# Optimization experiments

Measured on AMD Instinct MI355X. Metric: run time of the kernel, lower is better.

The kernel has to match this reference:

```python
import jax, jax.numpy as jnp
import numpy as np

N_NODES = 50000
N_EDGES = 640000
D = 128
L = 3


def setup_inputs() -> dict:
    key = jax.random.key(0)
    k1, k2, k3, k4 = jax.random.split(key, 4)
    x = jax.random.normal(k1, (N_NODES, D), dtype=jnp.float32)
    # Glorot-ish scale so activations stay O(1) across 3 layers
    Ws = jax.random.normal(k2, (L, D, D), dtype=jnp.float32) * (1.0 / np.sqrt(D))
    bs = jnp.zeros((L, D), dtype=jnp.float32)
    edge_src = jax.random.randint(k3, (N_EDGES,), 0, N_NODES, dtype=jnp.int32)
    edge_dst = jax.random.randint(k4, (N_EDGES,), 0, N_NODES, dtype=jnp.int32)
    return {"x": x, "Ws": Ws, "bs": bs, "edge_src": edge_src, "edge_dst": edge_dst}


def reference(x, Ws, bs, edge_src, edge_dst):
    n = x.shape[0]
    ones = jnp.ones(edge_src.shape[0], dtype=x.dtype)
    # degrees, clamped to 1 as in dgl GraphConv(norm='both')
    deg_out = jnp.maximum(jax.ops.segment_sum(ones, edge_src, num_segments=n), 1.0)
    deg_in = jnp.maximum(jax.ops.segment_sum(ones, edge_dst, num_segments=n), 1.0)
    inv_sqrt_out = jax.lax.rsqrt(deg_out)[:, None]  # [N,1]
    inv_sqrt_in = jax.lax.rsqrt(deg_in)[:, None]    # [N,1]
    for l in range(Ws.shape[0]):
        h = x * inv_sqrt_out                         # src normalization
        msg = h[edge_src]                            # [E,D] gather
        agg = jax.ops.segment_sum(msg, edge_dst, num_segments=n)  # [N,D] scatter-add
        h = agg * inv_sqrt_in                        # dst normalization
        x = jax.nn.relu(h @ Ws[l] + bs[l])           # linear + ReLU
    return x
```

## Files before the change

### kernel.cpp

```cpp
#include <hip/hip_runtime.h>
#include <hip/hip_fp16.h>

typedef __attribute__((ext_vector_type(8))) _Float16 half8;
typedef __attribute__((ext_vector_type(4))) float f32x4;
typedef unsigned int u32;
typedef unsigned short u16;
typedef unsigned long long u64;

#define ELL_PAD 64


__global__ __launch_bounds__(256) void initpack(int* __restrict__ deg_out,
                                                int* __restrict__ deg_in,
                                                u32* __restrict__ xz0,
                                                u32* __restrict__ xz1,
                                                const float* __restrict__ Ws,
                                                _Float16* __restrict__ Whi,
                                                _Float16* __restrict__ Wlo,
                                                int N, int padU32, int zb, int packTotal) {
  int b = blockIdx.x;
  if (b < zb) {
    int i = b * 256 + threadIdx.x;
    if (i < N) { deg_out[i] = 0; deg_in[i] = 0; }
    if (b == 0) {
      for (int j = threadIdx.x; j < padU32; j += 256) { xz0[j] = 0; xz1[j] = 0; }
    }
    return;
  }
  int i = (b - zb) * 256 + threadIdx.x;
  if (i < packTotal) {
    int lane  = i & 63;
    int kstep = (i >> 6) & 3;
    int ntile = (i >> 8) & 7;
    int layer = i >> 11;
    int nn = ntile * 16 + (lane & 15);
    int k0 = kstep * 32 + (lane >> 4) * 8;
    const float* W = Ws + (size_t)layer * 128 * 128;
    size_t base = (size_t)i * 8;
    for (int j = 0; j < 8; j++) {
      float v = W[(k0 + j) * 128 + nn];
      _Float16 hi = (_Float16)v;
      Whi[base + j] = hi;
      Wlo[base + j] = (_Float16)(v - (float)hi);
    }
  }
}


__global__ __launch_bounds__(256) void build(const int* __restrict__ esrc,
                                             const int* __restrict__ edst,
                                             int* __restrict__ deg_out,
                                             int* __restrict__ deg_in,
                                             u16* __restrict__ ell, int E) {
  int i = blockIdx.x * 256 + threadIdx.x;
  if (i >= E) return;
  int s = esrc[i];
  int d = edst[i];
  atomicAdd(&deg_out[s], 1);
  int p = atomicAdd(&deg_in[d], 1);
  if (p < ELL_PAD) ell[(u32)d * ELL_PAD + (u32)p] = (u16)s;
}


__global__ __launch_bounds__(256) void xscale(const float* __restrict__ x,
                                              const int* __restrict__ deg_out,
                                              const int* __restrict__ deg_in,
                                              __half2* __restrict__ xh,
                                              u16* __restrict__ ell,
                                              int N, int n64) {
  int gid = blockIdx.x * 256 + threadIdx.x;
  if (gid >= n64) return;
  int row = gid >> 6;
  int d = deg_out[row]; if (d < 1) d = 1;
  float s = rsqrtf((float)d);
  float2 v = ((const float2*)x)[gid];
  xh[gid] = __floats2half2_rn(v.x * s, v.y * s);
  if ((gid & 63) == 0) {
    int c = deg_in[row];
    int l = c > ELL_PAD ? ELL_PAD : c;
    int t = (l + 3) & ~3;
    u16* ep = ell + (u32)row * ELL_PAD;
    for (int q = l; q < t; q++) ep[q] = (u16)N;
  }
}


__global__ __launch_bounds__(512) void layer16(const _Float16* __restrict__ xh,
                                               const int* __restrict__ deg_in,
                                               const u16* __restrict__ ell,
                                               const _Float16* __restrict__ Whi,
                                               const _Float16* __restrict__ Wlo,
                                               const float* __restrict__ bias,
                                               const int* __restrict__ deg_out,
                                               __half* __restrict__ out16,
                                               float* __restrict__ out32, int n) {
  __shared__ _Float16 As[16 * 136];
  const int wave = threadIdx.x >> 6;
  const int lane = threadIdx.x & 63;
  const int sub  = lane & 15;
  const int grp  = lane >> 4;
  const int sh   = grp << 4;
  const u32 sub16 = (u32)sub * 16u;
  const int rowBase = blockIdx.x * 16;
  const char* __restrict__ xb = (const char*)xh;

  {
    int r0 = rowBase + wave * 2, r1 = r0 + 1;
    int d0 = (r0 < n) ? deg_in[r0] : 0;
    int d1 = (r1 < n) ? deg_in[r1] : 0;
    int l0 = d0 > ELL_PAD ? ELL_PAD : d0;
    int l1 = d1 > ELL_PAD ? ELL_PAD : d1;
    int t0 = (l0 + 3) & ~3;
    int t1 = (l1 + 3) & ~3;
    const u16* ep0 = ell + (u32)(r0 < n ? r0 : 0) * ELL_PAD;
    const u16* ep1 = ell + (u32)(r1 < n ? r1 : 0) * ELL_PAD;

    float a0[8] = {0.f, 0.f, 0.f, 0.f, 0.f, 0.f, 0.f, 0.f};
    float a1[8] = {0.f, 0.f, 0.f, 0.f, 0.f, 0.f, 0.f, 0.f};

    int m = t0 < t1 ? t0 : t1;
    int e = 0;
    for (; e + 8 <= m; e += 8) {
      u64 wa0 = *(const u64*)&ep0[e];
      u64 wa1 = *(const u64*)&ep0[e + 4];
      u64 wb0 = *(const u64*)&ep1[e];
      u64 wb1 = *(const u64*)&ep1[e + 4];
      u32 ia0 = ((u32)(wa0 >> sh) & 0xFFFFu) * 256u + sub16;
      u32 ia1 = ((u32)(wa1 >> sh) & 0xFFFFu) * 256u + sub16;
      u32 ib0 = ((u32)(wb0 >> sh) & 0xFFFFu) * 256u + sub16;
      u32 ib1 = ((u32)(wb1 >> sh) & 0xFFFFu) * 256u + sub16;
      half8 va0 = *(const half8*)(xb + ia0);
      half8 va1 = *(const half8*)(xb + ia1);
      half8 vb0 = *(const half8*)(xb + ib0);
      half8 vb1 = *(const half8*)(xb + ib1);
#pragma unroll
      for (int j = 0; j < 8; j++) {
        a0[j] += (float)va0[j] + (float)va1[j];
        a1[j] += (float)vb0[j] + (float)vb1[j];
      }
    }
    for (; e < m; e += 4) {
      u64 wa = *(const u64*)&ep0[e];
      u64 wb = *(const u64*)&ep1[e];
      u32 ia = ((u32)(wa >> sh) & 0xFFFFu) * 256u + sub16;
      u32 ib = ((u32)(wb >> sh) & 0xFFFFu) * 256u + sub16;
      half8 va = *(const half8*)(xb + ia);
      half8 vb = *(const half8*)(xb + ib);
#pragma unroll
      for (int j = 0; j < 8; j++) { a0[j] += (float)va[j]; a1[j] += (float)vb[j]; }
    }
    for (int ea = m; ea < t0; ea += 4) {
      u64 wa = *(const u64*)&ep0[ea];
      u32 ia = ((u32)(wa >> sh) & 0xFFFFu) * 256u + sub16;
      half8 va = *(const half8*)(xb + ia);
#pragma unroll
      for (int j = 0; j < 8; j++) a0[j] += (float)va[j];
    }
    for (int eb = m; eb < t1; eb += 4) {
      u64 wb = *(const u64*)&ep1[eb];
      u32 ib = ((u32)(wb >> sh) & 0xFFFFu) * 256u + sub16;
      half8 vb = *(const half8*)(xb + ib);
#pragma unroll
      for (int j = 0; j < 8; j++) a1[j] += (float)vb[j];
    }

#pragma unroll
    for (int j = 0; j < 8; j++) {
      a0[j] += __shfl_xor(a0[j], 16, 64);
      a0[j] += __shfl_xor(a0[j], 32, 64);
      a1[j] += __shfl_xor(a1[j], 16, 64);
      a1[j] += __shfl_xor(a1[j], 32, 64);
    }

    float si0 = rsqrtf((float)(d0 < 1 ? 1 : d0));
    float si1 = rsqrtf((float)(d1 < 1 ? 1 : d1));
    if (grp == 0) {
      half8 h0, h1;
#pragma unroll
      for (int j = 0; j < 8; j++) {
        h0[j] = (_Float16)(a0[j] * si0);
        h1[j] = (_Float16)(a1[j] * si1);
      }
      *(half8*)&As[(wave * 2 + 0) * 136 + sub * 8] = h0;
      *(half8*)&As[(wave * 2 + 1) * 136 + sub * 8] = h1;
    }
  }
  __syncthreads();

  f32x4 acc = (f32x4){0.f, 0.f, 0.f, 0.f};
#pragma unroll
  for (int ks = 0; ks < 4; ks++) {
    half8 a  = *(const half8*)&As[(size_t)sub * 136 + ks * 32 + grp * 8];
    half8 bh = *(const half8*)&Whi[((wave * 4 + ks) * 64 + lane) * 8];
    half8 bl = *(const half8*)&Wlo[((wave * 4 + ks) * 64 + lane) * 8];
    acc = __builtin_amdgcn_mfma_f32_16x16x32_f16(a, bh, acc, 0, 0, 0);
    acc = __builtin_amdgcn_mfma_f32_16x16x32_f16(a, bl, acc, 0, 0, 0);
  }

  const int r0c = rowBase + grp * 4;
  const int col = wave * 16 + sub;
  const float bv = bias[col];
#pragma unroll
  for (int r = 0; r < 4; r++) {
    int row = r0c + r;
    if (row < n) {
      float v = fmaxf(acc[r] + bv, 0.f);
      if (out16) {
        int d = deg_out[row]; if (d < 1) d = 1;
        out16[(size_t)row * 128 + col] = __float2half(v * rsqrtf((float)d));
      } else {
        out32[(size_t)row * 128 + col] = v;
      }
    }
  }
}


extern "C" void kernel_launch(void* const* d_in, const int* in_sizes, int n_in,
                              void* d_out, int out_size, void* d_ws, size_t ws_size,
                              hipStream_t stream) {
  const float* x   = (const float*)d_in[0];
  const float* Ws  = (const float*)d_in[1];
  const float* bs  = (const float*)d_in[2];
  const int* esrc  = (const int*)d_in[3];
  const int* edst  = (const int*)d_in[4];

  const int D = 128;
  const int N = in_sizes[0] / D;
  const int E = in_sizes[3];
  const int L = in_sizes[1] / (D * D);
  const int Npad = ((N + 15) / 16) * 16;

  char* base = (char*)d_ws;
  size_t off = 0;
  auto alloc = [&](size_t bytes) {
    char* p = base + off;
    off = (off + bytes + 255) & ~(size_t)255;
    return p;
  };
  int*      deg_out = (int*)alloc((size_t)N * 4);
  int*      deg_in  = (int*)alloc((size_t)N * 4);
  u16*      ell     = (u16*)alloc((size_t)N * ELL_PAD * 2);
  _Float16* Whi     = (_Float16*)alloc((size_t)L * 16384 * 2);
  _Float16* Wlo     = (_Float16*)alloc((size_t)L * 16384 * 2);
  _Float16* xh0     = (_Float16*)alloc((size_t)(Npad + 16) * 128 * 2);
  _Float16* xh1     = (_Float16*)alloc((size_t)(Npad + 16) * 128 * 2);

  const int zb = (N + 255) / 256;
  const int packTotal = L * 2048;
  const int packB = (packTotal + 255) / 256;
  const int padU32 = 16 * 64;

  initpack<<<dim3(zb + packB), dim3(256), 0, stream>>>(
      deg_out, deg_in,
      (u32*)(xh0 + (size_t)N * 128), (u32*)(xh1 + (size_t)N * 128),
      Ws, Whi, Wlo, N, padU32, zb, packTotal);
  build<<<dim3((E + 255) / 256), dim3(256), 0, stream>>>(
      esrc, edst, deg_out, deg_in, ell, E);
  xscale<<<dim3((N * 64 + 255) / 256), dim3(256), 0, stream>>>(
      x, deg_out, deg_in, (__half2*)xh0, ell, N, N * 64);

  float* outf = (float*)d_out;
  _Float16* ping[2] = {xh0, xh1};
  const dim3 lgrid(Npad / 16), lblk(512);

  for (int l = 0; l < L; l++) {
    bool last = (l == L - 1);
    layer16<<<lgrid, lblk, 0, stream>>>(
        (const _Float16*)ping[l & 1], deg_in, ell,
        Whi + (size_t)l * 16384, Wlo + (size_t)l * 16384,
        bs + (size_t)l * D, deg_out,
        last ? nullptr : (__half*)ping[(l + 1) & 1],
        last ? outf : nullptr, N);
  }
}
```

Baseline: 262.6 us.

## Build ELL adjacency via two-pass bucketed partition instead of global atomics

Replaces the single build kernel, which did global atomics on deg_in and scattered 16-bit ELL writes, with a two-pass partition. Pass one bins edges by destination bucket in shared memory and records per-block run offsets. Pass two assembles each 128-node bucket's ELL slice in LDS and writes it out coalesced, padding unused slots with N. This removes contended global atomics and scattered stores but adds an extra kernel, intermediate buffers and serial single-thread prefix scans.

New measurement: 250.8 us. -4.5%, faster.

```diff
diff --git a/kernel.cpp b/kernel.cpp
--- a/kernel.cpp
+++ b/kernel.cpp
@@ -8,10 +8,13 @@
 typedef unsigned long long u64;
 
 #define ELL_PAD 64
+#define BKT 128
+#define BKT_SH 7
+#define EPB 2048
+#define NAMAX 512
 
 
 __global__ __launch_bounds__(256) void initpack(int* __restrict__ deg_out,
-                                                int* __restrict__ deg_in,
                                                 u32* __restrict__ xz0,
                                                 u32* __restrict__ xz1,
                                                 const float* __restrict__ Ws,
@@ -21,7 +24,7 @@
   int b = blockIdx.x;
   if (b < zb) {
     int i = b * 256 + threadIdx.x;
-    if (i < N) { deg_out[i] = 0; deg_in[i] = 0; }
+    if (i < N) deg_out[i] = 0;
     if (b == 0) {
       for (int j = threadIdx.x; j < padU32; j += 256) { xz0[j] = 0; xz1[j] = 0; }
     }
@@ -47,27 +50,102 @@
 }
 
 
-__global__ __launch_bounds__(256) void build(const int* __restrict__ esrc,
+__global__ __launch_bounds__(256) void parta(const int* __restrict__ esrc,
                                              const int* __restrict__ edst,
                                              int* __restrict__ deg_out,
+                                             u32* __restrict__ part,
+                                             u32* __restrict__ runTab,
+                                             int E, int NB) {
+  __shared__ u32 hist[1024];
+  __shared__ u32 stage[EPB];
+  int a = blockIdx.x;
+  int e0 = a * EPB;
+  int e1 = min(E, e0 + EPB);
+  int len = e1 - e0;
+  for (int j = threadIdx.x; j <= NB; j += 256) hist[j] = 0;
+  __syncthreads();
+  for (int i = e0 + threadIdx.x; i < e1; i += 256) {
+    int s = esrc[i];
+    int d = edst[i];
+    atomicAdd(&deg_out[s], 1);
+    atomicAdd(&hist[d >> BKT_SH], 1u);
+  }
+  __syncthreads();
+  if (threadIdx.x == 0) {
+    u32 run = 0;
+    for (int b = 0; b < NB; b++) { u32 t = hist[b]; hist[b] = run; run += t; }
+  }
+  __syncthreads();
+  u32* rt = runTab + (size_t)a * (NB + 1);
+  for (int b = threadIdx.x; b < NB; b += 256) rt[b] = hist[b];
+  if (threadIdx.x == 0) rt[NB] = (u32)len;
+  __syncthreads();
+  for (int i = e0 + threadIdx.x; i < e1; i += 256) {
+    int s = esrc[i];
+    int d = edst[i];
+    u32 p = atomicAdd(&hist[d >> BKT_SH], 1u);
+    stage[p] = (u32)s | ((u32)(d & (BKT - 1)) << 16);
+  }
+  __syncthreads();
+  u32* op = part + (size_t)a * EPB;
+  for (int j = threadIdx.x; j < len; j += 256) op[j] = stage[j];
+}
+
+
+__global__ __launch_bounds__(256) void partb(const u32* __restrict__ part,
+                                             const u32* __restrict__ runTab,
                                              int* __restrict__ deg_in,
-                                             u16* __restrict__ ell, int E) {
-  int i = blockIdx.x * 256 + threadIdx.x;
-  if (i >= E) return;
-  int s = esrc[i];
-  int d = edst[i];
-  atomicAdd(&deg_out[s], 1);
-  int p = atomicAdd(&deg_in[d], 1);
-  if (p < ELL_PAD) ell[(u32)d * ELL_PAD + (u32)p] = (u16)s;
+                                             u16* __restrict__ ell,
+                                             int N, int NA, int NB) {
+  __shared__ u16 slice[BKT * ELL_PAD];
+  __shared__ u32 cnt[BKT];
+  __shared__ u32 roff[NAMAX + 1];
+  __shared__ u32 rbase[NAMAX];
+  int b = blockIdx.x;
+  int base = b * BKT;
+  int hi = min(BKT, N - base);
+  if (hi <= 0) return;
+
+  u32 nv = ((u32)N << 16) | (u32)N;
+  u32* s32 = (u32*)slice;
+  for (int j = threadIdx.x; j < BKT * (ELL_PAD / 2); j += 256) s32[j] = nv;
+  for (int j = threadIdx.x; j < BKT; j += 256) cnt[j] = 0;
+  for (int a = threadIdx.x; a < NA; a += 256) {
+    u32 s = runTab[(size_t)a * (NB + 1) + b];
+    u32 e = runTab[(size_t)a * (NB + 1) + b + 1];
+    roff[a]  = e - s;
+    rbase[a] = (u32)a * EPB + s;
+  }
+  __syncthreads();
+  if (threadIdx.x == 0) {
+    u32 run = 0;
+    for (int a = 0; a < NA; a++) { u32 t = roff[a]; roff[a] = run; run += t; }
+    roff[NA] = run;
+  }
+  __syncthreads();
+  int T = (int)roff[NA];
+  for (int i = threadIdx.x; i < T; i += 256) {
+    int lo = 0, hh = NA;
+    while (hh - lo > 1) {
+      int mid = (lo + hh) >> 1;
+      if (roff[mid] <= (u32)i) lo = mid; else hh = mid;
+    }
+    u32 pair = part[(size_t)rbase[lo] + ((u32)i - roff[lo])];
+    u32 dl  = pair >> 16;
+    u32 src = pair & 0xFFFFu;
+    u32 c = atomicAdd(&cnt[dl], 1u);
+    if (c < ELL_PAD) slice[dl * ELL_PAD + c] = (u16)src;
+  }
+  __syncthreads();
+  for (int t = threadIdx.x; t < hi; t += 256) deg_in[base + t] = (int)cnt[t];
+  u32* eg = (u32*)(ell + (size_t)base * ELL_PAD);
+  for (int j = threadIdx.x; j < hi * (ELL_PAD / 2); j += 256) eg[j] = s32[j];
 }
 
 
 __global__ __launch_bounds__(256) void xscale(const float* __restrict__ x,
                                               const int* __restrict__ deg_out,
-                                              const int* __restrict__ deg_in,
-                                              __half2* __restrict__ xh,
-                                              u16* __restrict__ ell,
-                                              int N, int n64) {
+                                              __half2* __restrict__ xh, int n64) {
   int gid = blockIdx.x * 256 + threadIdx.x;
   if (gid >= n64) return;
   int row = gid >> 6;
@@ -75,13 +153,6 @@
   float s = rsqrtf((float)d);
   float2 v = ((const float2*)x)[gid];
   xh[gid] = __floats2half2_rn(v.x * s, v.y * s);
-  if ((gid & 63) == 0) {
-    int c = deg_in[row];
-    int l = c > ELL_PAD ? ELL_PAD : c;
-    int t = (l + 3) & ~3;
-    u16* ep = ell + (u32)row * ELL_PAD;
-    for (int q = l; q < t; q++) ep[q] = (u16)N;
-  }
 }
 
 
@@ -230,6 +301,8 @@
   const int E = in_sizes[3];
   const int L = in_sizes[1] / (D * D);
   const int Npad = ((N + 15) / 16) * 16;
+  const int NA = (E + EPB - 1) / EPB;
+  const int NB = (N + BKT - 1) / BKT;
 
   char* base = (char*)d_ws;
   size_t off = 0;
@@ -245,6 +318,8 @@
   _Float16* Wlo     = (_Float16*)alloc((size_t)L * 16384 * 2);
   _Float16* xh0     = (_Float16*)alloc((size_t)(Npad + 16) * 128 * 2);
   _Float16* xh1     = (_Float16*)alloc((size_t)(Npad + 16) * 128 * 2);
+  u32*      part    = (u32*)alloc((size_t)NA * EPB * 4);
+  u32*      runTab  = (u32*)alloc((size_t)NA * (NB + 1) * 4);
 
   const int zb = (N + 255) / 256;
   const int packTotal = L * 2048;
@@ -252,13 +327,15 @@
   const int padU32 = 16 * 64;
 
   initpack<<<dim3(zb + packB), dim3(256), 0, stream>>>(
-      deg_out, deg_in,
+      deg_out,
       (u32*)(xh0 + (size_t)N * 128), (u32*)(xh1 + (size_t)N * 128),
       Ws, Whi, Wlo, N, padU32, zb, packTotal);
-  build<<<dim3((E + 255) / 256), dim3(256), 0, stream>>>(
-      esrc, edst, deg_out, deg_in, ell, E);
+  parta<<<dim3(NA), dim3(256), 0, stream>>>(
+      esrc, edst, deg_out, part, runTab, E, NB);
+  partb<<<dim3(NB), dim3(256), 0, stream>>>(
+      part, runTab, deg_in, ell, N, NA, NB);
   xscale<<<dim3((N * 64 + 255) / 256), dim3(256), 0, stream>>>(
-      x, deg_out, deg_in, (__half2*)xh0, ell, N, N * 64);
+      x, deg_out, (__half2*)xh0, N * 64);
 
   float* outf = (float*)d_out;
   _Float16* ping[2] = {xh0, xh1};
```
